# Performance work log

Hardware: AMD Instinct MI355X
Metric: run time of the kernel (lower is better)

The kernel has to match this reference:

```python
import jax, jax.numpy as jnp
import numpy as np

B, C, W, H = 16, 256, 32, 32
HEADS = 4


def setup_inputs() -> dict:
    key = jax.random.key(0)
    ks = jax.random.split(key, 9)
    d = C // HEADS
    return {
        "x": jax.random.normal(ks[0], (B, C, W, H), jnp.float32),
        "Wq": jax.random.normal(ks[1], (C, C), jnp.float32) * 0.05,
        "bq": jax.random.normal(ks[2], (C,), jnp.float32) * 0.05,
        "Wk": jax.random.normal(ks[3], (C, C), jnp.float32) * 0.05,
        "bk": jax.random.normal(ks[4], (C,), jnp.float32) * 0.05,
        "Wv": jax.random.normal(ks[5], (C, C), jnp.float32) * 0.05,
        "bv": jax.random.normal(ks[6], (C,), jnp.float32) * 0.05,
        "rel_h": jax.random.normal(ks[7], (1, HEADS, d, 1, H), jnp.float32),
        "rel_w": jax.random.normal(ks[8], (1, HEADS, d, W, 1), jnp.float32),
    }


def reference(x, Wq, bq, Wk, bk, Wv, bv, rel_h, rel_w):
    b, c, w, h = x.shape
    heads = rel_h.shape[1]
    d = c // heads
    n = w * h  # sequence length = spatial positions
    xf = x.reshape(b, c, n)

    def proj(Wt, bt):
        # 1x1 conv == per-position linear over channels
        y = jnp.einsum('oc,bcn->bon', Wt, xf) + bt[None, :, None]
        return y.reshape(b, heads, d, n)

    q = proj(Wq, bq)
    k = proj(Wk, bk)
    v = proj(Wv, bv)

    # similarity = q^T k : [b, heads, n, n]
    sim = jnp.einsum('bhdi,bhdj->bhij', q, k)
    # relative position bias content term: rel^T q
    rel = (rel_h + rel_w).reshape(heads, d, n)  # broadcast-add then flatten spatial
    qpos = jnp.einsum('hdi,bhdj->bhij', rel, q)

    attn = jax.nn.softmax(sim + qpos, axis=-1)
    # out = v @ attn^T : [b, heads, d, n]
    out = jnp.einsum('bhdn,bhmn->bhdm', v, attn)
    return out.reshape(b, c, w, h)
```

## Files before the change

### kernel.cpp

```cpp
#include <hip/hip_runtime.h>

constexpr int Bb  = 16;
constexpr int Cch = 256;
constexpr int NH  = 4;
constexpr int Dh  = 64;
constexpr int Nn  = 1024;

typedef _Float16 f16;
typedef __attribute__((ext_vector_type(8))) _Float16 f16x8;
typedef __attribute__((ext_vector_type(4))) _Float16 f16x4;
typedef __attribute__((ext_vector_type(4))) float    f32x4;

__global__ __launch_bounds__(256) void prep_kernel(
    const float* __restrict__ x,
    const float* __restrict__ Wq, const float* __restrict__ Wk,
    const float* __restrict__ Wv,
    const float* __restrict__ rel_h, const float* __restrict__ rel_w,
    f16* __restrict__ xt, f16* __restrict__ Wh, f16* __restrict__ rel_t)
{
    const int gx = blockIdx.x;
    const int t  = threadIdx.x;
    __shared__ float T[64][65];

    if (gx < 1024) {
        const int n0 = (gx & 15) * 64;
        const int c0 = ((gx >> 4) & 3) * 64;
        const int b  = gx >> 6;
        #pragma unroll
        for (int rep = 0; rep < 16; rep++) {
            const int e  = t + rep * 256;
            const int r  = e >> 6;
            const int cc = e & 63;
            T[r][cc] = x[((size_t)b * Cch + c0 + r) * Nn + n0 + cc];
        }
        __syncthreads();
        #pragma unroll
        for (int rep = 0; rep < 4; rep++) {
            const int e  = t + rep * 256;
            const int nn = e >> 4;
            const int c4 = e & 15;
            f16x4 w;
            w.x = (f16)T[c4 * 4 + 0][nn];
            w.y = (f16)T[c4 * 4 + 1][nn];
            w.z = (f16)T[c4 * 4 + 2][nn];
            w.w = (f16)T[c4 * 4 + 3][nn];
            *(f16x4*)&xt[((size_t)b * Nn + n0 + nn) * Cch + c0 + c4 * 4] = w;
        }
    } else if (gx < 2048) {
        const int idx = (gx - 1024) * 256 + t;
        const int d = idx & 63;
        const int n = (idx >> 6) & (Nn - 1);
        const int h = idx >> 16;
        const int hd = h * 64 + d;
        rel_t[idx] = (f16)(rel_h[hd * 32 + (n & 31)] + rel_w[hd * 32 + (n >> 5)]);
    } else {
        const int idx = (gx - 2048) * 256 + t;
        const int og  = idx >> 8;
        const int c   = idx & 255;
        const int p   = og >> 8;
        const int o   = og & 255;
        const float* W = (p == 0) ? Wq : (p == 1) ? Wk : Wv;
        Wh[idx] = (f16)W[o * 256 + c];
    }
}

__global__ __launch_bounds__(256) void gemm_qkv(
    const f16* __restrict__ Wh, const f16* __restrict__ xt,
    const float* __restrict__ bq, const float* __restrict__ bk,
    const float* __restrict__ bv,
    f16* __restrict__ qt, f16* __restrict__ kt, f16* __restrict__ vb)
{
    const int bx   = blockIdx.x;
    const int y    = blockIdx.y;
    const int b    = blockIdx.z;
    const int p    = y >> 1;
    const int half = y & 1;

    constexpr int ST = 40;
    __shared__ f16 Wt[128 * ST];
    __shared__ f16 Xt[128 * ST];

    const int t    = threadIdx.x;
    const int wave = t >> 6;
    const int lane = t & 63;
    const int l16  = lane & 15;
    const int quad = lane >> 4;
    const int wm   = wave >> 1;
    const int wsd  = wave & 1;

    f32x4 acc[4][4];
    #pragma unroll
    for (int mi = 0; mi < 4; mi++)
        #pragma unroll
        for (int ni = 0; ni < 4; ni++) acc[mi][ni] = (f32x4){0.f, 0.f, 0.f, 0.f};

    const f16* Wg = Wh + (size_t)y * 128 * 256;
    const f16* Xg = xt + ((size_t)b * Nn + bx * 128) * 256;

    for (int c0 = 0; c0 < 256; c0 += 32) {
        f16x8 wch[2], xch[2];
        #pragma unroll
        for (int rep = 0; rep < 2; rep++) {
            const int e   = t + rep * 256;
            const int row = e >> 2;
            const int c8  = e & 3;
            wch[rep] = *(const f16x8*)&Wg[(size_t)row * 256 + c0 + c8 * 8];
            xch[rep] = *(const f16x8*)&Xg[(size_t)row * 256 + c0 + c8 * 8];
        }
        __syncthreads();
        #pragma unroll
        for (int rep = 0; rep < 2; rep++) {
            const int e   = t + rep * 256;
            const int row = e >> 2;
            const int c8  = e & 3;
            *(f16x8*)&Wt[row * ST + c8 * 8] = wch[rep];
            *(f16x8*)&Xt[row * ST + c8 * 8] = xch[rep];
        }
        __syncthreads();

        const f16* tf = (p < 2) ? Wt : Xt;
        const f16* ts = (p < 2) ? Xt : Wt;
        f16x8 af[4], bf[4];
        #pragma unroll
        for (int mi = 0; mi < 4; mi++)
            af[mi] = *(const f16x8*)&tf[(wm * 64 + mi * 16 + l16) * ST + quad * 8];
        #pragma unroll
        for (int ni = 0; ni < 4; ni++)
            bf[ni] = *(const f16x8*)&ts[(wsd * 64 + ni * 16 + l16) * ST + quad * 8];
        #pragma unroll
        for (int mi = 0; mi < 4; mi++)
            #pragma unroll
            for (int ni = 0; ni < 4; ni++)
                acc[mi][ni] = __builtin_amdgcn_mfma_f32_16x16x32_f16(
                    af[mi], bf[ni], acc[mi][ni], 0, 0, 0);
    }

    if (p < 2) {
        f16* yt = (p == 0) ? qt : kt;
        const float* bg = (p == 0) ? bq : bk;
        #pragma unroll
        for (int mi = 0; mi < 4; mi++) {
            const int o_in = half * 128 + wm * 64 + mi * 16 + quad * 4;
            const float4 b4 = *(const float4*)&bg[o_in];
            const int h = o_in >> 6;
            const int d = o_in & 63;
            #pragma unroll
            for (int ni = 0; ni < 4; ni++) {
                const int n = bx * 128 + wsd * 64 + ni * 16 + l16;
                f16x4 w;
                w.x = (f16)(acc[mi][ni][0] + b4.x);
                w.y = (f16)(acc[mi][ni][1] + b4.y);
                w.z = (f16)(acc[mi][ni][2] + b4.z);
                w.w = (f16)(acc[mi][ni][3] + b4.w);
                *(f16x4*)&yt[(((size_t)b * NH + h) * Nn + n) * Dh + d] = w;
            }
        }
    } else {
        #pragma unroll
        for (int ni = 0; ni < 4; ni++) {
            const int c  = half * 128 + wsd * 64 + ni * 16 + l16;
            const float bs = bv[c];
            #pragma unroll
            for (int mi = 0; mi < 4; mi++) {
                const int n = bx * 128 + wm * 64 + mi * 16 + quad * 4;
                f16x4 w;
                w.x = (f16)(acc[mi][ni][0] + bs);
                w.y = (f16)(acc[mi][ni][1] + bs);
                w.z = (f16)(acc[mi][ni][2] + bs);
                w.w = (f16)(acc[mi][ni][3] + bs);
                *(f16x4*)&vb[((size_t)b * Cch + c) * Nn + n] = w;
            }
        }
    }
}

__global__ __launch_bounds__(512, 4) void attn_mfma(
    const f16* __restrict__ qt, const f16* __restrict__ kt,
    const f16* __restrict__ relt, const f16* __restrict__ vb,
    float* __restrict__ out)
{
    const int bid = blockIdx.x;
    const int bh  = bid & 63;
    const int i0  = (bid >> 6) * 128;
    const int h   = bh & 3;
    const int b   = bh >> 2;

    const f16* qtb = qt  + (size_t)bh * Nn * Dh;
    const f16* ktb = kt  + (size_t)bh * Nn * Dh;
    const f16* rlt = relt + (size_t)h * Nn * Dh;
    const f16* vbb = vb  + (size_t)(b * Cch + h * Dh) * Nn;

    __shared__ f16 Qa_s[128 * 128];
    __shared__ f16 Ka_s[64 * 128];
    __shared__ f16 v_s [64 * 64];
    __shared__ f16 Pt_s[128 * 64];

    const int t    = threadIdx.x;
    const int wave = t >> 6;
    const int lane = t & 63;
    const int l16  = lane & 15;
    const int quad = lane >> 4;

    #pragma unroll
    for (int rep = 0; rep < 4; rep++) {
        const int e   = t + rep * 512;
        const int row = e >> 4;
        const int c8  = e & 15;
        const f16* src = (c8 < 8)
            ? &qtb[(size_t)(i0 + row) * Dh + c8 * 8]
            : &rlt[(size_t)(i0 + row) * Dh + (c8 - 8) * 8];
        *(f16x8*)&Qa_s[(row << 7) + ((c8 ^ (row & 7)) << 3)] = *(const f16x8*)src;
    }
    __syncthreads();

    f16x8 af[4];
    {
        const int row = wave * 16 + l16;
        #pragma unroll
        for (int k = 0; k < 4; k++)
            af[k] = *(const f16x8*)
                &Qa_s[(row << 7) + ((((k << 2) + quad) ^ (row & 7)) << 3)];
    }

    f16x8 ones;
    #pragma unroll
    for (int u = 0; u < 8; u++) ones[u] = (f16)1.0f;

    f32x4 Of[4], Ol;
    float m_r[4];
    Ol = (f32x4){0.f, 0.f, 0.f, 0.f};
    #pragma unroll
    for (int ds = 0; ds < 4; ds++) Of[ds] = (f32x4){0.f, 0.f, 0.f, 0.f};
    #pragma unroll
    for (int r = 0; r < 4; r++) m_r[r] = -1e30f;

    for (int j0 = 0; j0 < Nn; j0 += 64) {
        f16x8 kreg[2], vreg;
        #pragma unroll
        for (int rep = 0; rep < 2; rep++) {
            const int e   = t + rep * 512;
            const int row = e >> 4;
            const int c8  = e & 15;
            const f16* src = (c8 < 8)
                ? &ktb[(size_t)(j0 + row) * Dh + c8 * 8]
                : &qtb[(size_t)(j0 + row) * Dh + (c8 - 8) * 8];
            kreg[rep] = *(const f16x8*)src;
        }
        {
            const int row = t >> 3;
            const int c8  = t & 7;
            vreg = *(const f16x8*)&vbb[(size_t)row * Nn + j0 + c8 * 8];
        }

        __syncthreads();
        #pragma unroll
        for (int rep = 0; rep < 2; rep++) {
            const int e   = t + rep * 512;
            const int row = e >> 4;
            const int c8  = e & 15;
            *(f16x8*)&Ka_s[(row << 7) + ((c8 ^ (row & 7)) << 3)] = kreg[rep];
        }
        {
            const int row = t >> 3;
            const int c8  = t & 7;
            *(f16x8*)&v_s[(row << 6) + ((c8 ^ (row & 7)) << 3)] = vreg;
        }
        __syncthreads();

        f32x4 Sf[4];
        #pragma unroll
        for (int js = 0; js < 4; js++) Sf[js] = (f32x4){0.f, 0.f, 0.f, 0.f};
        #pragma unroll
        for (int k = 0; k < 4; k++) {
            f16x8 bb[4];
            #pragma unroll
            for (int js = 0; js < 4; js++) {
                const int row = js * 16 + l16;
                bb[js] = *(const f16x8*)
                    &Ka_s[(row << 7) + ((((k << 2) + quad) ^ (row & 7)) << 3)];
            }
            #pragma unroll
            for (int js = 0; js < 4; js++)
                Sf[js] = __builtin_amdgcn_mfma_f32_16x16x32_f16(
                    af[k], bb[js], Sf[js], 0, 0, 0);
        }

        #pragma unroll
        for (int r = 0; r < 4; r++) {
            float tm = fmaxf(fmaxf(Sf[0][r], Sf[1][r]),
                             fmaxf(Sf[2][r], Sf[3][r]));
            tm = fmaxf(tm, __shfl_xor(tm, 1));
            tm = fmaxf(tm, __shfl_xor(tm, 2));
            tm = fmaxf(tm, __shfl_xor(tm, 4));
            tm = fmaxf(tm, __shfl_xor(tm, 8));
            const float mnew  = fmaxf(m_r[r], tm);
            const float alpha = __expf(m_r[r] - mnew);
            m_r[r] = mnew;

            const int row = wave * 16 + quad * 4 + r;
            const int rx  = row & 7;
            #pragma unroll
            for (int js = 0; js < 4; js++) {
                const float p = __expf(Sf[js][r] - mnew);
                const int col = js * 16 + l16;
                Pt_s[(row << 6) + (((col >> 3) ^ rx) << 3) + (col & 7)] = (f16)p;
            }
            #pragma unroll
            for (int ds = 0; ds < 4; ds++) Of[ds][r] *= alpha;
            Ol[r] *= alpha;
        }

        #pragma unroll
        for (int ks = 0; ks < 2; ks++) {
            const int prow = wave * 16 + l16;
            f16x8 pa = *(const f16x8*)
                &Pt_s[(prow << 6) + ((((ks << 2) + quad) ^ (prow & 7)) << 3)];
            #pragma unroll
            for (int ds = 0; ds < 4; ds++) {
                const int vrow = ds * 16 + l16;
                f16x8 vv = *(const f16x8*)
                    &v_s[(vrow << 6) + ((((ks << 2) + quad) ^ (vrow & 7)) << 3)];
                Of[ds] = __builtin_amdgcn_mfma_f32_16x16x32_f16(
                    pa, vv, Of[ds], 0, 0, 0);
            }
            Ol = __builtin_amdgcn_mfma_f32_16x16x32_f16(
                pa, ones, Ol, 0, 0, 0);
        }
    }

    #pragma unroll
    for (int r = 0; r < 4; r++) {
        const float inv = 1.0f / Ol[r];
        const int i = i0 + wave * 16 + quad * 4 + r;
        #pragma unroll
        for (int ds = 0; ds < 4; ds++) {
            const int d = ds * 16 + l16;
            out[((size_t)(b * Cch + h * Dh + d)) * Nn + i] = Of[ds][r] * inv;
        }
    }
}

extern "C" void kernel_launch(void* const* d_in, const int* in_sizes, int n_in,
                              void* d_out, int out_size, void* d_ws, size_t ws_size,
                              hipStream_t stream)
{
    const float* x     = (const float*)d_in[0];
    const float* Wq    = (const float*)d_in[1];
    const float* bq    = (const float*)d_in[2];
    const float* Wk    = (const float*)d_in[3];
    const float* bk    = (const float*)d_in[4];
    const float* Wv    = (const float*)d_in[5];
    const float* bv    = (const float*)d_in[6];
    const float* rel_h = (const float*)d_in[7];
    const float* rel_w = (const float*)d_in[8];

    f16* ws = (f16*)d_ws;
    const size_t SZQ = (size_t)Bb * NH * Nn * Dh;
    f16* qt   = ws;
    f16* kt   = ws + SZQ;
    f16* vbuf = ws + 2 * SZQ;
    f16* relt = ws + 3 * SZQ;
    f16* xth  = ws + 3 * SZQ + (size_t)NH * Nn * Dh;
    f16* Wh   = xth + SZQ;

    prep_kernel<<<dim3(2816), 256, 0, stream>>>(
        x, Wq, Wk, Wv, rel_h, rel_w, xth, Wh, relt);
    gemm_qkv<<<dim3(Nn / 128, 6, Bb), 256, 0, stream>>>(
        Wh, xth, bq, bk, bv, qt, kt, vbuf);
    attn_mfma<<<dim3(512), 512, 0, stream>>>(
        qt, kt, relt, vbuf, (float*)d_out);
}
```

Before: 160.1 us.

## Fuse x transpose and weight fp16 cast into QKV GEMM loads

The QKV projection GEMM now reads fp32 x and weights directly, converting to fp16 and transposing x through an extra shared-memory staging tile inside the K loop. This removes the separate prep pass that wrote transposed fp16 x and weights to workspace and the global round trip that went with it. The relative-position table gets its own small kernel that writes four elements per thread. In exchange, each GEMM block reads twice as many bytes per element, does its own casts, re-reads x once per output tile row, and needs an extra barrier per K step.

```diff
diff --git a/kernel.cpp b/kernel.cpp
--- a/kernel.cpp
+++ b/kernel.cpp
@@ -11,61 +11,27 @@
 typedef __attribute__((ext_vector_type(4))) _Float16 f16x4;
 typedef __attribute__((ext_vector_type(4))) float    f32x4;
 
-__global__ __launch_bounds__(256) void prep_kernel(
+__global__ __launch_bounds__(256) void prep_rel(
+    const float* __restrict__ rel_h, const float* __restrict__ rel_w,
+    f16* __restrict__ rel_t)
+{
+    const int idx0 = (blockIdx.x * 256 + threadIdx.x) * 4;
+    const int d0 = idx0 & 63;
+    const int n  = (idx0 >> 6) & (Nn - 1);
+    const int h  = idx0 >> 16;
+    f16x4 w;
+    #pragma unroll
+    for (int u = 0; u < 4; u++) {
+        const int hd = h * 64 + d0 + u;
+        w[u] = (f16)(rel_h[hd * 32 + (n & 31)] + rel_w[hd * 32 + (n >> 5)]);
+    }
+    *(f16x4*)&rel_t[idx0] = w;
+}
+
+__global__ __launch_bounds__(256) void gemm_qkv(
     const float* __restrict__ x,
     const float* __restrict__ Wq, const float* __restrict__ Wk,
     const float* __restrict__ Wv,
-    const float* __restrict__ rel_h, const float* __restrict__ rel_w,
-    f16* __restrict__ xt, f16* __restrict__ Wh, f16* __restrict__ rel_t)
-{
-    const int gx = blockIdx.x;
-    const int t  = threadIdx.x;
-    __shared__ float T[64][65];
-
-    if (gx < 1024) {
-        const int n0 = (gx & 15) * 64;
-        const int c0 = ((gx >> 4) & 3) * 64;
-        const int b  = gx >> 6;
-        #pragma unroll
-        for (int rep = 0; rep < 16; rep++) {
-            const int e  = t + rep * 256;
-            const int r  = e >> 6;
-            const int cc = e & 63;
-            T[r][cc] = x[((size_t)b * Cch + c0 + r) * Nn + n0 + cc];
-        }
-        __syncthreads();
-        #pragma unroll
-        for (int rep = 0; rep < 4; rep++) {
-            const int e  = t + rep * 256;
-            const int nn = e >> 4;
-            const int c4 = e & 15;
-            f16x4 w;
-            w.x = (f16)T[c4 * 4 + 0][nn];
-            w.y = (f16)T[c4 * 4 + 1][nn];
-            w.z = (f16)T[c4 * 4 + 2][nn];
-            w.w = (f16)T[c4 * 4 + 3][nn];
-            *(f16x4*)&xt[((size_t)b * Nn + n0 + nn) * Cch + c0 + c4 * 4] = w;
-        }
-    } else if (gx < 2048) {
-        const int idx = (gx - 1024) * 256 + t;
-        const int d = idx & 63;
-        const int n = (idx >> 6) & (Nn - 1);
-        const int h = idx >> 16;
-        const int hd = h * 64 + d;
-        rel_t[idx] = (f16)(rel_h[hd * 32 + (n & 31)] + rel_w[hd * 32 + (n >> 5)]);
-    } else {
-        const int idx = (gx - 2048) * 256 + t;
-        const int og  = idx >> 8;
-        const int c   = idx & 255;
-        const int p   = og >> 8;
-        const int o   = og & 255;
-        const float* W = (p == 0) ? Wq : (p == 1) ? Wk : Wv;
-        Wh[idx] = (f16)W[o * 256 + c];
-    }
-}
-
-__global__ __launch_bounds__(256) void gemm_qkv(
-    const f16* __restrict__ Wh, const f16* __restrict__ xt,
     const float* __restrict__ bq, const float* __restrict__ bk,
     const float* __restrict__ bv,
     f16* __restrict__ qt, f16* __restrict__ kt, f16* __restrict__ vb)
@@ -77,8 +43,9 @@
     const int half = y & 1;
 
     constexpr int ST = 40;
-    __shared__ f16 Wt[128 * ST];
-    __shared__ f16 Xt[128 * ST];
+    __shared__ f16   Wt[128 * ST];
+    __shared__ f16   Xt[128 * ST];
+    __shared__ float T [32 * 132];
 
     const int t    = threadIdx.x;
     const int wave = t >> 6;
@@ -88,33 +55,55 @@
     const int wm   = wave >> 1;
     const int wsd  = wave & 1;
 
+    const float* Wsel = (p == 0) ? Wq : (p == 1) ? Wk : Wv;
+
     f32x4 acc[4][4];
     #pragma unroll
     for (int mi = 0; mi < 4; mi++)
         #pragma unroll
         for (int ni = 0; ni < 4; ni++) acc[mi][ni] = (f32x4){0.f, 0.f, 0.f, 0.f};
 
-    const f16* Wg = Wh + (size_t)y * 128 * 256;
-    const f16* Xg = xt + ((size_t)b * Nn + bx * 128) * 256;
-
     for (int c0 = 0; c0 < 256; c0 += 32) {
-        f16x8 wch[2], xch[2];
+        float4 wreg[4], xreg[4];
+        #pragma unroll
+        for (int rep = 0; rep < 4; rep++) {
+            const int e  = t + rep * 256;
+            const int r  = e >> 3;
+            const int c4 = e & 7;
+            wreg[rep] = *(const float4*)
+                &Wsel[(size_t)(half * 128 + r) * 256 + c0 + c4 * 4];
+            const int cc = e >> 5;
+            const int n4 = e & 31;
+            xreg[rep] = *(const float4*)
+                &x[((size_t)b * Cch + c0 + cc) * Nn + bx * 128 + n4 * 4];
+        }
+        __syncthreads();
+
+        #pragma unroll
+        for (int rep = 0; rep < 4; rep++) {
+            const int e  = t + rep * 256;
+            const int r  = e >> 3;
+            const int c4 = e & 7;
+            f16x4 wv;
+            wv.x = (f16)wreg[rep].x; wv.y = (f16)wreg[rep].y;
+            wv.z = (f16)wreg[rep].z; wv.w = (f16)wreg[rep].w;
+            *(f16x4*)&Wt[r * ST + c4 * 4] = wv;
+            const int cc = e >> 5;
+            const int n4 = e & 31;
+            *(float4*)&T[cc * 132 + n4 * 4] = xreg[rep];
+        }
+        __syncthreads();
+
         #pragma unroll
         for (int rep = 0; rep < 2; rep++) {
-            const int e   = t + rep * 256;
-            const int row = e >> 2;
-            const int c8  = e & 3;
-            wch[rep] = *(const f16x8*)&Wg[(size_t)row * 256 + c0 + c8 * 8];
-            xch[rep] = *(const f16x8*)&Xg[(size_t)row * 256 + c0 + c8 * 8];
-        }
-        __syncthreads();
-        #pragma unroll
-        for (int rep = 0; rep < 2; rep++) {
-            const int e   = t + rep * 256;
-            const int row = e >> 2;
-            const int c8  = e & 3;
-            *(f16x8*)&Wt[row * ST + c8 * 8] = wch[rep];
-            *(f16x8*)&Xt[row * ST + c8 * 8] = xch[rep];
+            const int e  = t + rep * 256;
+            const int nn = e & 127;
+            const int c8 = e >> 7;
+            f16x8 xv;
+            #pragma unroll
+            for (int u = 0; u < 8; u++)
+                xv[u] = (f16)T[(c8 * 8 + u) * 132 + nn];
+            *(f16x8*)&Xt[nn * ST + c8 * 8] = xv;
         }
         __syncthreads();
 
@@ -360,13 +349,10 @@
     f16* kt   = ws + SZQ;
     f16* vbuf = ws + 2 * SZQ;
     f16* relt = ws + 3 * SZQ;
-    f16* xth  = ws + 3 * SZQ + (size_t)NH * Nn * Dh;
-    f16* Wh   = xth + SZQ;
-
-    prep_kernel<<<dim3(2816), 256, 0, stream>>>(
-        x, Wq, Wk, Wv, rel_h, rel_w, xth, Wh, relt);
+
+    prep_rel<<<dim3(256), 256, 0, stream>>>(rel_h, rel_w, relt);
     gemm_qkv<<<dim3(Nn / 128, 6, Bb), 256, 0, stream>>>(
-        Wh, xth, bq, bk, bv, qt, kt, vbuf);
+        x, Wq, Wk, Wv, bq, bk, bv, qt, kt, vbuf);
     attn_mfma<<<dim3(512), 512, 0, stream>>>(
         qt, kt, relt, vbuf, (float*)d_out);
 }
```

New measurement: 181.6 us. +13.4%, slower.
